# Kernel tuning notes

Measured on AMD Instinct MI355X. Metric: run time of the kernel, lower is better.

## Reference

```python
import jax, jax.numpy as jnp
import numpy as np

N_NODES = 100000
N_EDGES = 20000
NNZ = 1600000
D_IN = 128
D_OUT = 128
STAR = 64
NEG_SLOPE = 0.2


def setup_inputs() -> dict:
    key = jax.random.key(0)
    ks = jax.random.split(key, 10)
    X = jax.random.normal(ks[0], (N_NODES, D_IN), dtype=jnp.float32)
    V = jax.random.randint(ks[1], (NNZ,), 0, N_NODES, dtype=jnp.int32)
    E = jax.random.randint(ks[2], (NNZ,), 0, N_EDGES, dtype=jnp.int32)
    # guarantee full index range coverage (torch infers sizes via .max()+1)
    V = V.at[0].set(N_NODES - 1)
    E = E.at[0].set(N_EDGES - 1)
    S_features = jax.random.normal(ks[3], (N_EDGES, STAR), dtype=jnp.float32)
    # linear layer params (PyTorch convention: weight [out, in])
    def lin(k, fan_out, fan_in):
        bound = 1.0 / np.sqrt(fan_in)
        return jax.random.uniform(k, (fan_out, fan_in), jnp.float32, -bound, bound)
    Wx_w = lin(ks[4], D_OUT, D_IN)
    Wx_b = jnp.zeros((D_OUT,), jnp.float32)
    Wv_w = lin(ks[5], D_OUT, D_IN)
    Wv_b = jnp.zeros((D_OUT,), jnp.float32)
    a_w = lin(ks[6], 1, D_OUT)
    Wt_w = lin(ks[7], D_OUT, D_OUT + STAR)
    Wt_b = jnp.zeros((D_OUT,), jnp.float32)
    return {"X": X, "V": V, "E": E, "S_features": S_features,
            "Wx_w": Wx_w, "Wx_b": Wx_b, "Wv_w": Wv_w, "Wv_b": Wv_b,
            "a_w": a_w, "Wt_w": Wt_w, "Wt_b": Wt_b}


def reference(X, V, E, S_features, Wx_w, Wx_b, Wv_w, Wv_b, a_w, Wt_w, Wt_b):
    X_init = X @ Wx_w.T + Wx_b                      # [N, D_OUT]
    X_feat = X @ Wv_w.T + Wv_b                      # [N, D_OUT]
    score = (X_feat @ a_w.T)[:, 0]                  # [N]
    s = jax.nn.leaky_relu(score[V], NEG_SLOPE)      # [nnz], gather
    # scatter_softmax over hyperedge groups E
    m = jax.ops.segment_max(s, E, num_segments=N_EDGES)
    w = jnp.exp(s - m[E])
    denom = jax.ops.segment_sum(w, E, num_segments=N_EDGES)
    soft = w / denom[E]                             # [nnz]
    Xev = X_feat[V] * soft[:, None]                 # [nnz, D_OUT]
    Y_v2e = jax.nn.elu(jax.ops.segment_sum(Xev, E, num_segments=N_EDGES))
    e_msg = jnp.concatenate([Y_v2e, S_features], axis=1)  # [Eg, D_OUT+STAR]
    Y = e_msg @ Wt_w.T + Wt_b                       # [Eg, D_OUT]
    Yev = Y[E]                                      # [nnz, D_OUT]
    cnt = jax.ops.segment_sum(jnp.ones((Yev.shape[0],), X.dtype), V, num_segments=N_NODES)
    Xm = jax.ops.segment_sum(Yev, V, num_segments=N_NODES) / jnp.maximum(cnt, 1.0)[:, None]
    Xm = jax.nn.elu(Xm)  # is_last=False; dropout rate 0 -> no-op
    return Xm + X_init
```

## Files before the change

kernel.cpp:

```cpp
#include <hip/hip_runtime.h>
#include <hip/hip_bf16.h>
#include <hip/hip_fp16.h>

#define N_NODES 100000
#define N_EDGES 20000
#define NNZ     1600000
#define D       128
#define STAR    64
#define NEG_SLOPE 0.2f

#define NBLK_E  400
#define CHUNK_E 4000
#define H32_E   10000

#define NBLK_N  64
#define CHUNK_N 25000
#define BINS_N  20000
#define H32_N   10000
#define NPASS_N 5

#define NGRP    8
#define CPG_E   (NBLK_E / NGRP)
#define CPG_N   (NBLK_N / NGRP)

#define SCAT_NWG ((NNZ + 255) / 256)
#define SCAT_Q   (SCAT_NWG / 8)
#define SCAT_R   (SCAT_NWG % 8)

#define TGB_E ((N_EDGES + 255) / 256)
#define TGB_N ((N_NODES + 255) / 256)

#define SCC 16
#define SC_PER_BLOCK (256 * SCC)
#define SCB_E ((N_EDGES + SC_PER_BLOCK - 1) / SC_PER_BLOCK)
#define SCB_N ((N_NODES + SC_PER_BLOCK - 1) / SC_PER_BLOCK)

typedef _Float16 half8 __attribute__((ext_vector_type(8)));
typedef float    floatx4 __attribute__((ext_vector_type(4)));

__device__ __forceinline__ float elu_fast(float t)
{
    return (t > 0.f) ? t : (__expf(t) - 1.f);
}

__device__ __forceinline__ half8 cvt8(float4 f0, float4 f1)
{
    half8 h;
    h[0] = (_Float16)f0.x; h[1] = (_Float16)f0.y;
    h[2] = (_Float16)f0.z; h[3] = (_Float16)f0.w;
    h[4] = (_Float16)f1.x; h[5] = (_Float16)f1.y;
    h[6] = (_Float16)f1.z; h[7] = (_Float16)f1.w;
    return h;
}

__global__ __launch_bounds__(256) void k_cvt_w(
    const float* __restrict__ Wx, const float* __restrict__ Wv,
    const float* __restrict__ Wt,
    __half* __restrict__ Wf16, __half* __restrict__ Wtf16)
{
    int i = (blockIdx.x * 256 + threadIdx.x) * 4;
    const float* src;
    __half* dst;
    if (i < 16384)            { src = Wx + i;         dst = Wf16 + i; }
    else if (i < 32768)       { src = Wv + (i-16384); dst = Wf16 + i; }
    else if (i < 32768+24576) { src = Wt + (i-32768); dst = Wtf16 + (i-32768); }
    else return;
    float4 f = *(const float4*)src;
    *(__half2*)(dst)     = __floats2half2_rn(f.x, f.y);
    *(__half2*)(dst + 2) = __floats2half2_rn(f.z, f.w);
}

__global__ __launch_bounds__(256) void k_node_gemm(
    const float* __restrict__ X, const __half* __restrict__ Wf16,
    const float* __restrict__ Wxb, const float* __restrict__ Wvb,
    const float* __restrict__ aw,
    float* __restrict__ Xinit, __half* __restrict__ Xf16,
    float* __restrict__ wexp)
{
    __shared__ char smem[64 * 256];
    const int tid  = threadIdx.x;
    const int w    = tid >> 6;
    const int lane = tid & 63;
    const int bm   = blockIdx.x * 64;
    const int colbase = w * 64;
    const bool isInit = (colbase < D);
    const int r16 = lane & 15;
    const int hi  = lane >> 4;
    const int g8  = hi * 8;

    {
        const int r  = tid >> 2;
        int srow = bm + r; if (srow >= N_NODES) srow = N_NODES - 1;
        const float4* src = (const float4*)(X + (size_t)srow * D + (tid & 3) * 32);
        float4 f[8];
        #pragma unroll
        for (int j = 0; j < 8; ++j) f[j] = src[j];
        const int swz  = (r & 7) << 4;
        const int base = r * 256 + (tid & 3) * 64;
        #pragma unroll
        for (int j = 0; j < 4; ++j)
            *(half8*)(smem + ((base + j * 16) ^ swz)) = cvt8(f[2*j], f[2*j+1]);
    }

    half8 bf[4][4];
    #pragma unroll
    for (int ks = 0; ks < 4; ++ks)
        #pragma unroll
        for (int n = 0; n < 4; ++n)
            bf[ks][n] = *(const half8*)(Wf16 + (size_t)(colbase + n*16 + r16) * D
                                        + ks * 32 + g8);

    __syncthreads();

    floatx4 acc[4][4] = {};
    #pragma unroll
    for (int ks = 0; ks < 4; ++ks) {
        half8 a[4];
        #pragma unroll
        for (int m = 0; m < 4; ++m) {
            const int R = m * 16 + r16;
            a[m] = *(const half8*)(smem + ((R*256 + ks*64 + hi*16) ^ ((R&7)<<4)));
        }
        #pragma unroll
        for (int m = 0; m < 4; ++m)
            #pragma unroll
            for (int n = 0; n < 4; ++n)
                acc[m][n] = __builtin_amdgcn_mfma_f32_16x16x32_f16(
                    bf[ks][n], a[m], acc[m][n], 0, 0, 0);
    }

    const float* bias = isInit ? Wxb : Wvb;

    __syncthreads();

    if (isInit) {
        #pragma unroll
        for (int n = 0; n < 4; ++n) {
            const int c4 = (colbase & (D - 1)) + n * 16 + hi * 4;
            float4 bb = *(const float4*)(bias + c4);
            #pragma unroll
            for (int m = 0; m < 4; ++m) {
                const int row = bm + m * 16 + r16;
                if (row < N_NODES) {
                    float4 o = make_float4(acc[m][n][0] + bb.x, acc[m][n][1] + bb.y,
                                           acc[m][n][2] + bb.z, acc[m][n][3] + bb.w);
                    *(float4*)(Xinit + (size_t)row * D + c4) = o;
                }
            }
        }
    } else {
        #pragma unroll
        for (int n = 0; n < 4; ++n) {
            const int c4 = (colbase & (D - 1)) + n * 16 + hi * 4;
            float4 bb = *(const float4*)(bias + c4);
            const int lcb = ((colbase - D) + n * 16 + hi * 4) * 2;
            #pragma unroll
            for (int m = 0; m < 4; ++m) {
                const int row = m * 16 + r16;
                char* dst = smem + row * 256 + (lcb ^ ((row & 7) << 4));
                *(__half2*)(dst)     = __floats2half2_rn(acc[m][n][0] + bb.x,
                                                         acc[m][n][1] + bb.y);
                *(__half2*)(dst + 4) = __floats2half2_rn(acc[m][n][2] + bb.z,
                                                         acc[m][n][3] + bb.w);
            }
        }
    }
    __syncthreads();
    {
        const int r   = tid >> 2;
        const int row = bm + r;
        const int q4  = tid & 3;
        if (row < N_NODES) {
            const int swz = (r & 7) << 4;
            __half* dst = Xf16 + (size_t)row * D + q4 * 32;
            float part = 0.f;
            #pragma unroll
            for (int j = 0; j < 4; ++j) {
                half8 h = *(const half8*)(smem + r * 256 + ((q4 * 64 + j * 16) ^ swz));
                *(half8*)(dst + j * 8) = h;
                float4 a0 = *(const float4*)(aw + q4 * 32 + j * 8);
                float4 a1 = *(const float4*)(aw + q4 * 32 + j * 8 + 4);
                part += (float)h[0]*a0.x + (float)h[1]*a0.y
                      + (float)h[2]*a0.z + (float)h[3]*a0.w
                      + (float)h[4]*a1.x + (float)h[5]*a1.y
                      + (float)h[6]*a1.z + (float)h[7]*a1.w;
            }
            part += __shfl_xor(part, 1, 64);
            part += __shfl_xor(part, 2, 64);
            if (q4 == 0) {
                float l = (part > 0.f) ? part : NEG_SLOPE * part;
                wexp[row] = expf(l);
            }
        }
    }
}

__global__ __launch_bounds__(256) void k_part_all(
    const int* __restrict__ E, const int* __restrict__ V,
    unsigned short* __restrict__ part_e, unsigned short* __restrict__ part_n,
    unsigned short* __restrict__ re, unsigned short* __restrict__ rn)
{
    __shared__ int h[H32_E];
    const int blk = blockIdx.x;
    for (int t = threadIdx.x; t < H32_E; t += 256) h[t] = 0;
    __syncthreads();

    if (blk < NBLK_E) {
        const int b = blk;
        const int i0 = b * CHUNK_E;
        const int4* E4 = (const int4*)(E + i0);
        for (int i = threadIdx.x; i < CHUNK_E / 4; i += 256) {
            int4 q = E4[i];
            int ev[4] = {q.x, q.y, q.z, q.w};
            #pragma unroll
            for (int t = 0; t < 4; ++t) {
                int e = ev[t];
                unsigned sh = (e & 1) << 4;
                int old = atomicAdd(&h[e >> 1], 1 << sh);
                re[i0 + i * 4 + t] = (unsigned short)((unsigned)old >> sh);
            }
        }
        __syncthreads();
        int* dst = (int*)(part_e + (size_t)b * N_EDGES);
        for (int t = threadIdx.x; t < H32_E; t += 256) dst[t] = h[t];
    } else {
        const int idx = blk - NBLK_E;
        const int b   = idx & 63;
        const int c0  = (idx >> 6) * BINS_N;
        const int i0  = b * CHUNK_N;
        const int4* V4 = (const int4*)(V + i0);
        for (int i = threadIdx.x; i < CHUNK_N / 4; i += 256) {
            int4 q = V4[i];
            int vv[4] = {q.x, q.y, q.z, q.w};
            #pragma unroll
            for (int t = 0; t < 4; ++t) {
                int c = vv[t] - c0;
                if ((unsigned)c < (unsigned)BINS_N) {
                    unsigned sh = (c & 1) << 4;
                    int old = atomicAdd(&h[c >> 1], 1 << sh);
                    rn[i0 + i * 4 + t] = (unsigned short)((unsigned)old >> sh);
                }
            }
        }
        __syncthreads();
        int* dst = (int*)(part_n + (size_t)b * N_NODES + c0);
        for (int t = threadIdx.x; t < H32_N; t += 256) dst[t] = h[t];
    }
}

__global__ __launch_bounds__(256) void k_tot_grp2(
    unsigned short* __restrict__ part_e, int* __restrict__ gsum_e,
    unsigned short* __restrict__ part_n, int* __restrict__ gsum_n)
{
    const int g = blockIdx.y;
    unsigned short* part; int* gsum; int nbins, cpg, bin;
    if (blockIdx.x < TGB_E) {
        bin = blockIdx.x * 256 + threadIdx.x;
        part = part_e; gsum = gsum_e; nbins = N_EDGES; cpg = CPG_E;
    } else {
        bin = (blockIdx.x - TGB_E) * 256 + threadIdx.x;
        part = part_n; gsum = gsum_n; nbins = N_NODES; cpg = CPG_N;
    }
    if (bin >= nbins) return;
    int run = 0;
    #pragma unroll 8
    for (int b = g * cpg; b < (g + 1) * cpg; ++b) {
        size_t idx = (size_t)b * nbins + bin;
        int v = part[idx];
        part[idx] = (unsigned short)run;
        run += v;
    }
    gsum[(size_t)g * nbins + bin] = run;
}

__global__ __launch_bounds__(256) void k_tot_fin2(
    int* __restrict__ gsum_e, int* __restrict__ tot_e,
    int* __restrict__ gsum_n, int* __restrict__ tot_n)
{
    int* gsum; int* tot; int nbins, bin;
    if (blockIdx.x < TGB_E) {
        bin = blockIdx.x * 256 + threadIdx.x;
        gsum = gsum_e; tot = tot_e; nbins = N_EDGES;
    } else {
        bin = (blockIdx.x - TGB_E) * 256 + threadIdx.x;
        gsum = gsum_n; tot = tot_n; nbins = N_NODES;
    }
    if (bin >= nbins) return;
    int run = 0;
    #pragma unroll
    for (int g = 0; g < NGRP; ++g) {
        size_t idx = (size_t)g * nbins + bin;
        int v = gsum[idx];
        gsum[idx] = run;
        run += v;
    }
    tot[bin] = run;
}

__global__ __launch_bounds__(256) void k_scan_bsum2(
    const int* __restrict__ tot_e, int* __restrict__ bsum_e,
    const int* __restrict__ tot_n, int* __restrict__ bsum_n)
{
    __shared__ int red[256];
    const int* cnt; int* bsum; int n, blk;
    if (blockIdx.x < SCB_E) { cnt = tot_e; bsum = bsum_e; n = N_EDGES; blk = blockIdx.x; }
    else { cnt = tot_n; bsum = bsum_n; n = N_NODES; blk = blockIdx.x - SCB_E; }
    const int base = blk * SC_PER_BLOCK + threadIdx.x * SCC;
    int s = 0;
    if (base + SCC <= n) {
        const int4* p4 = (const int4*)(cnt + base);
        #pragma unroll
        for (int j = 0; j < SCC / 4; ++j) {
            int4 v = p4[j];
            s += v.x + v.y + v.z + v.w;
        }
    } else {
        for (int i = base; i < n; ++i) s += cnt[i];
    }
    red[threadIdx.x] = s;
    __syncthreads();
    for (int d = 128; d > 0; d >>= 1) {
        if (threadIdx.x < d) red[threadIdx.x] += red[threadIdx.x + d];
        __syncthreads();
    }
    if (threadIdx.x == 0) bsum[blk] = red[0];
}

__global__ __launch_bounds__(1024) void k_scan_bbase2(
    int* __restrict__ bsum_e, int* __restrict__ eoff,
    int* __restrict__ bsum_n, int* __restrict__ noff)
{
    __shared__ int sums[1024];
    int* bsum; int* off; int nb, n;
    if (blockIdx.x == 0) { bsum = bsum_e; off = eoff; nb = SCB_E; n = N_EDGES; }
    else                 { bsum = bsum_n; off = noff; nb = SCB_N; n = N_NODES; }
    const int tid = threadIdx.x;
    sums[tid] = (tid < nb) ? bsum[tid] : 0;
    __syncthreads();
    for (int d = 1; d < 1024; d <<= 1) {
        int mine = sums[tid];
        int other = (tid >= d) ? sums[tid - d] : 0;
        __syncthreads();
        sums[tid] = mine + other;
        __syncthreads();
    }
    if (tid < nb) bsum[tid] = (tid > 0) ? sums[tid - 1] : 0;
    if (tid == 0) off[n] = sums[1023];
}

__global__ __launch_bounds__(256) void k_scan_out2(
    const int* __restrict__ tot_e, const int* __restrict__ bsum_e,
    int* __restrict__ eoff,
    const int* __restrict__ tot_n, const int* __restrict__ bsum_n,
    int* __restrict__ noff)
{
    __shared__ int tsum[256];
    const int* cnt; const int* bsum; int* off; int n, blk;
    if (blockIdx.x < SCB_E) {
        cnt = tot_e; bsum = bsum_e; off = eoff; n = N_EDGES; blk = blockIdx.x;
    } else {
        cnt = tot_n; bsum = bsum_n; off = noff; n = N_NODES; blk = blockIdx.x - SCB_E;
    }
    const int base = blk * SC_PER_BLOCK + threadIdx.x * SCC;
    int vals[SCC];
    int s = 0;
    if (base + SCC <= n) {
        const int4* p4 = (const int4*)(cnt + base);
        #pragma unroll
        for (int j = 0; j < SCC / 4; ++j) {
            int4 v = p4[j];
            vals[4 * j + 0] = v.x; vals[4 * j + 1] = v.y;
            vals[4 * j + 2] = v.z; vals[4 * j + 3] = v.w;
            s += v.x + v.y + v.z + v.w;
        }
    } else {
        #pragma unroll
        for (int j = 0; j < SCC; ++j) {
            int i = base + j;
            vals[j] = (i < n) ? cnt[i] : 0;
            s += vals[j];
        }
    }
    tsum[threadIdx.x] = s;
    __syncthreads();
    for (int d = 1; d < 256; d <<= 1) {
        int mine = tsum[threadIdx.x];
        int other = (threadIdx.x >= d) ? tsum[threadIdx.x - d] : 0;
        __syncthreads();
        tsum[threadIdx.x] = mine + other;
        __syncthreads();
    }
    int run = bsum[blk] + ((threadIdx.x > 0) ? tsum[threadIdx.x - 1] : 0);
    #pragma unroll
    for (int j = 0; j < SCC; ++j) {
        int i = base + j;
        if (i < n) { off[i] = run; run += vals[j]; }
    }
}

__global__ __launch_bounds__(256) void k_scatter_both(
    const int* __restrict__ V, const int* __restrict__ E,
    const unsigned short* __restrict__ re, const unsigned short* __restrict__ rn,
    const unsigned short* __restrict__ part_e,
    const unsigned short* __restrict__ part_n,
    const int* __restrict__ gsum_e, const int* __restrict__ gsum_n,
    const int* __restrict__ eoff, const int* __restrict__ noff,
    int* __restrict__ epairs, unsigned short* __restrict__ nedges)
{
    const int bid = blockIdx.x;
    const int xcd = bid & 7;
    const int j   = bid >> 3;
    const int vb  = (xcd < SCAT_R) ? xcd * (SCAT_Q + 1) + j
                                   : SCAT_R * (SCAT_Q + 1) + (xcd - SCAT_R) * SCAT_Q + j;
    int i = vb * 256 + (int)threadIdx.x;
    if (i >= NNZ) return;
    int e = E[i], v = V[i];
    int be = i / CHUNK_E;
    int bn = i / CHUNK_N;
    int g  = i / 200000;
    int pe = eoff[e] + gsum_e[(size_t)g * N_EDGES + e]
                     + part_e[(size_t)be * N_EDGES + e] + re[i];
    int pn = noff[v] + gsum_n[(size_t)g * N_NODES + v]
                     + part_n[(size_t)bn * N_NODES + v] + rn[i];
    epairs[pe] = v;
    nedges[pn] = (unsigned short)e;
}

__device__ __forceinline__ void acc8h(float w, float4 raw, float (&a)[8])
{
    const __half2* h = (const __half2*)&raw;
    #pragma unroll
    for (int t = 0; t < 4; ++t) {
        float2 f = __half22float2(h[t]);
        a[2*t]   = fmaf(w, f.x, a[2*t]);
        a[2*t+1] = fmaf(w, f.y, a[2*t+1]);
    }
}

__global__ __launch_bounds__(256) void k_edge_agg(
    const int* __restrict__ epairs, const int* __restrict__ eoff,
    const float* __restrict__ wexp,
    const __half* __restrict__ Xf16, const float* __restrict__ S,
    float* __restrict__ emsg)
{
    const int wave = threadIdx.x >> 6, lane = threadIdx.x & 63;
    const int e = blockIdx.x * 4 + wave;
    if (e >= N_EDGES) return;
    const int beg = eoff[e], end = eoff[e + 1];
    const int slot = lane >> 4;
    const int sl = lane & 15;
    float a[8] = {};
    float dsum = 0.f;
    int j = beg;
    for (; j + 15 < end; j += 16) {
        int v0 = epairs[j + slot];
        int v1 = epairs[j + 4 + slot];
        int v2 = epairs[j + 8 + slot];
        int v3 = epairs[j + 12 + slot];
        float w0 = wexp[v0], w1 = wexp[v1], w2 = wexp[v2], w3 = wexp[v3];
        float4 r0 = *(const float4*)(Xf16 + (size_t)v0 * D + sl * 8);
        float4 r1 = *(const float4*)(Xf16 + (size_t)v1 * D + sl * 8);
        float4 r2 = *(const float4*)(Xf16 + (size_t)v2 * D + sl * 8);
        float4 r3 = *(const float4*)(Xf16 + (size_t)v3 * D + sl * 8);
        dsum += (w0 + w1) + (w2 + w3);
        acc8h(w0, r0, a);
        acc8h(w1, r1, a);
        acc8h(w2, r2, a);
        acc8h(w3, r3, a);
    }
    for (; j + 3 < end; j += 4) {
        int v = epairs[j + slot];
        float w = wexp[v];
        float4 r = *(const float4*)(Xf16 + (size_t)v * D + sl * 8);
        dsum += w;
        acc8h(w, r, a);
    }
    if (j + slot < end) {
        int v = epairs[j + slot];
        float w = wexp[v];
        float4 r = *(const float4*)(Xf16 + (size_t)v * D + sl * 8);
        dsum += w;
        acc8h(w, r, a);
    }
    #pragma unroll
    for (int k = 0; k < 8; ++k) {
        a[k] += __shfl_xor(a[k], 16, 64);
        a[k] += __shfl_xor(a[k], 32, 64);
    }
    dsum += __shfl_xor(dsum, 16, 64);
    dsum += __shfl_xor(dsum, 32, 64);

    float inv = (end > beg) ? 1.f / dsum : 0.f;
    float y[8];
    #pragma unroll
    for (int k = 0; k < 8; ++k)
        y[k] = elu_fast(a[k] * inv);
    const size_t rb = (size_t)e * (D + STAR);
    if (slot == 0) {
        *(float4*)(emsg + rb + sl * 8)     = make_float4(y[0], y[1], y[2], y[3]);
        *(float4*)(emsg + rb + sl * 8 + 4) = make_float4(y[4], y[5], y[6], y[7]);
    } else if (slot == 1) {
        float4 s4 = *(const float4*)(S + (size_t)e * STAR + sl * 4);
        *(float4*)(emsg + rb + D + sl * 4) = s4;
    }
}

__global__ __launch_bounds__(256) void k_edge_gemm(
    const float* __restrict__ A, const __half* __restrict__ Wtf16,
    const float* __restrict__ Wtb, __half* __restrict__ Y16)
{
    __shared__ char smem[64 * 384];
    const int KDIM = D + STAR;
    const int tid  = threadIdx.x;
    const int w    = tid >> 6;
    const int lane = tid & 63;
    const int bm   = blockIdx.x * 64;
    const int colbase = w * 32;
    const int r16 = lane & 15;
    const int hi  = lane >> 4;
    const int g8  = hi * 8;

    {
        const int r = tid >> 2;
        int srow = bm + r; if (srow >= N_EDGES) srow = N_EDGES - 1;
        const float4* src = (const float4*)(A + (size_t)srow * KDIM + (tid & 3) * 48);
        float4 f[12];
        #pragma unroll
        for (int j = 0; j < 12; ++j) f[j] = src[j];
        const int swz  = (r & 7) << 4;
        const int base = r * 384 + (tid & 3) * 96;
        #pragma unroll
        for (int j = 0; j < 6; ++j)
            *(half8*)(smem + ((base + j * 16) ^ swz)) = cvt8(f[2*j], f[2*j+1]);
    }

    half8 bf[6][2];
    #pragma unroll
    for (int ks = 0; ks < 6; ++ks)
        #pragma unroll
        for (int n = 0; n < 2; ++n)
            bf[ks][n] = *(const half8*)(Wtf16 + (size_t)(colbase + n*16 + r16) * KDIM
                                        + ks * 32 + g8);

    __syncthreads();

    floatx4 acc[4][2] = {};
    #pragma unroll
    for (int ks = 0; ks < 6; ++ks) {
        half8 a[4];
        #pragma unroll
        for (int m = 0; m < 4; ++m) {
            const int R = m * 16 + r16;
            a[m] = *(const half8*)(smem + ((R*384 + ks*64 + hi*16) ^ ((R&7)<<4)));
        }
        #pragma unroll
        for (int m = 0; m < 4; ++m)
            #pragma unroll
            for (int n = 0; n < 2; ++n)
                acc[m][n] = __builtin_amdgcn_mfma_f32_16x16x32_f16(
                    a[m], bf[ks][n], acc[m][n], 0, 0, 0);
    }

    const int rq = hi * 4;
    __syncthreads();

    {
        __half* sh = (__half*)smem;
        #pragma unroll
        for (int n = 0; n < 2; ++n) {
            const int c = colbase + n * 16 + r16;
            const float bv = Wtb[c];
            #pragma unroll
            for (int m = 0; m < 4; ++m)
                #pragma unroll
                for (int q = 0; q < 4; ++q)
                    sh[(m * 16 + rq + q) * 128 + c] =
                        __float2half(acc[m][n][q] + bv);
        }
    }
    __syncthreads();
    {
        const int r   = tid >> 2;
        const int row = bm + r;
        if (row < N_EDGES) {
            const char* src = smem + r * 256 + (tid & 3) * 64;
            __half* dst = Y16 + (size_t)row * D + (tid & 3) * 32;
            #pragma unroll
            for (int j = 0; j < 4; ++j)
                *(half8*)(dst + j * 8) = *(const half8*)(src + j * 16);
        }
    }
}

__global__ __launch_bounds__(256) void k_node_agg(
    const unsigned short* __restrict__ nedges, const int* __restrict__ noff,
    const __half* __restrict__ Y16, float* __restrict__ out)
{
    const int wave = threadIdx.x >> 6, lane = threadIdx.x & 63;
    const int v = blockIdx.x * 4 + wave;
    if (v >= N_NODES) return;
    const int beg = noff[v], end = noff[v + 1];
    const int slot = lane >> 4;
    const int sl = lane & 15;
    float a[8] = {};
    int j = beg;
    for (; j + 7 < end; j += 8) {
        int e0 = nedges[j + slot];
        int e1 = nedges[j + 4 + slot];
        float4 r0 = *(const float4*)(Y16 + (size_t)e0 * D + sl * 8);
        float4 r1 = *(const float4*)(Y16 + (size_t)e1 * D + sl * 8);
        acc8h(1.f, r0, a);
        acc8h(1.f, r1, a);
    }
    for (; j + 3 < end; j += 4) {
        int e0 = nedges[j + slot];
        float4 r = *(const float4*)(Y16 + (size_t)e0 * D + sl * 8);
        acc8h(1.f, r, a);
    }
    if (j + slot < end) {
        int e0 = nedges[j + slot];
        float4 r = *(const float4*)(Y16 + (size_t)e0 * D + sl * 8);
        acc8h(1.f, r, a);
    }
    #pragma unroll
    for (int k = 0; k < 8; ++k) {
        a[k] += __shfl_xor(a[k], 16, 64);
        a[k] += __shfl_xor(a[k], 32, 64);
    }

    if (slot == 0) {
        int cnt = end - beg;
        float invc = 1.f / (float)max(cnt, 1);
        float x[8];
        #pragma unroll
        for (int k = 0; k < 8; ++k)
            x[k] = elu_fast(a[k] * invc);
        float4* o0 = (float4*)(out + (size_t)v * D + sl * 8);
        float4* o1 = (float4*)(out + (size_t)v * D + sl * 8 + 4);
        float4 c0 = *o0, c1 = *o1;
        *o0 = make_float4(c0.x + x[0], c0.y + x[1], c0.z + x[2], c0.w + x[3]);
        *o1 = make_float4(c1.x + x[4], c1.y + x[5], c1.z + x[6], c1.w + x[7]);
    }
}

extern "C" void kernel_launch(void* const* d_in, const int* in_sizes, int n_in,
                              void* d_out, int out_size, void* d_ws, size_t ws_size,
                              hipStream_t stream)
{
    const float* X    = (const float*)d_in[0];
    const int*   V    = (const int*)  d_in[1];
    const int*   E    = (const int*)  d_in[2];
    const float* S    = (const float*)d_in[3];
    const float* Wx_w = (const float*)d_in[4];
    const float* Wx_b = (const float*)d_in[5];
    const float* Wv_w = (const float*)d_in[6];
    const float* Wv_b = (const float*)d_in[7];
    const float* a_w  = (const float*)d_in[8];
    const float* Wt_w = (const float*)d_in[9];
    const float* Wt_b = (const float*)d_in[10];
    float* out = (float*)d_out;

    char* p = (char*)d_ws;
    auto take = [&](size_t bytes) -> char* {
        char* r = p;
        p += (bytes + 255) & ~(size_t)255;
        return r;
    };

    __half* Xf16  = (__half*)take((size_t)N_NODES * D * 2);
    float*  wexp  = (float*) take((size_t)N_NODES * 4);
    unsigned short* part_e = (unsigned short*)take((size_t)NBLK_E * N_EDGES * 2);
    unsigned short* part_n = (unsigned short*)take((size_t)NBLK_N * N_NODES * 2);
    int*    gsum_e = (int*)  take((size_t)NGRP * N_EDGES * 4);
    int*    gsum_n = (int*)  take((size_t)NGRP * N_NODES * 4);
    int*    tot_e = (int*)   take((size_t)N_EDGES * 4);
    int*    tot_n = (int*)   take((size_t)N_NODES * 4);
    int*    eoff  = (int*)   take((size_t)(N_EDGES + 1) * 4);
    int*    noff  = (int*)   take((size_t)(N_NODES + 1) * 4);
    int*    bsum_e = (int*)  take((size_t)SCB_E * 4);
    int*    bsum_n = (int*)  take((size_t)SCB_N * 4);
    unsigned short* re = (unsigned short*)take((size_t)NNZ * 2);
    unsigned short* rn = (unsigned short*)take((size_t)NNZ * 2);
    int*    epairs = (int*)  take((size_t)NNZ * 4);
    unsigned short* nedges = (unsigned short*)take((size_t)NNZ * 2);
    float*  emsg  = (float*) take((size_t)N_EDGES * (D + STAR) * 4);
    __half* Y16   = (__half*)take((size_t)N_EDGES * D * 2);
    __half* Wf16  = (__half*)take((size_t)256 * D * 2);
    __half* Wtf16 = (__half*)take((size_t)D * (D + STAR) * 2);

    k_cvt_w<<<56, 256, 0, stream>>>(Wx_w, Wv_w, Wt_w, Wf16, Wtf16);

    k_node_gemm<<<(N_NODES + 63) / 64, 256, 0, stream>>>(
        X, Wf16, Wx_b, Wv_b, a_w, out, Xf16, wexp);

    k_part_all<<<NBLK_E + NBLK_N * NPASS_N, 256, 0, stream>>>(
        E, V, part_e, part_n, re, rn);

    k_tot_grp2<<<dim3(TGB_E + TGB_N, NGRP), 256, 0, stream>>>(
        part_e, gsum_e, part_n, gsum_n);
    k_tot_fin2<<<TGB_E + TGB_N, 256, 0, stream>>>(
        gsum_e, tot_e, gsum_n, tot_n);
    k_scan_bsum2<<<SCB_E + SCB_N, 256, 0, stream>>>(
        tot_e, bsum_e, tot_n, bsum_n);
    k_scan_bbase2<<<2, 1024, 0, stream>>>(bsum_e, eoff, bsum_n, noff);
    k_scan_out2<<<SCB_E + SCB_N, 256, 0, stream>>>(
        tot_e, bsum_e, eoff, tot_n, bsum_n, noff);

    k_scatter_both<<<SCAT_NWG, 256, 0, stream>>>(
        V, E, re, rn, part_e, part_n, gsum_e, gsum_n,
        eoff, noff, epairs, nedges);

    k_edge_agg<<<(N_EDGES + 3) / 4, 256, 0, stream>>>(
        epairs, eoff, wexp, Xf16, S, emsg);

    k_edge_gemm<<<(N_EDGES + 63) / 64, 256, 0, stream>>>(emsg, Wtf16, Wt_b, Y16);

    k_node_agg<<<(N_NODES + 3) / 4, 256, 0, stream>>>(nedges, noff, Y16, out);
}
```

Measured before the change: 384.1 us.

## Split edge aggregation across four feature-column quarters per edge

Each edge's 128-wide aggregation is now split across four blocks, one per 32-column quarter. Within a wave, 16 nnz slots run in parallel with 4 lanes per quarter. The block index is remapped so the four quarter-blocks of the same edges are launched close together, which should help the shared epairs/wexp reads hit in cache. This adds parallelism and shortens the per-wave serial loop. In exchange, the index and weight loads are repeated four times and the shuffle reduction grows from two steps to four.

New measurement: 426.2 us. 11.0% more time.

```diff
diff --git a/kernel.cpp b/kernel.cpp
--- a/kernel.cpp
+++ b/kernel.cpp
@@ -26,6 +26,10 @@
 #define SCAT_NWG ((NNZ + 255) / 256)
 #define SCAT_Q   (SCAT_NWG / 8)
 #define SCAT_R   (SCAT_NWG % 8)
+
+#define EAGG_EB  (N_EDGES / 4)
+#define EAGG_NWG (4 * EAGG_EB)
+#define EAGG_HB  (EAGG_EB / 2)
 
 #define TGB_E ((N_EDGES + 255) / 256)
 #define TGB_N ((N_NODES + 255) / 256)
@@ -443,65 +447,73 @@
     const __half* __restrict__ Xf16, const float* __restrict__ S,
     float* __restrict__ emsg)
 {
+    const int k  = blockIdx.x & 7;
+    const int jb = blockIdx.x >> 3;
+    const int q  = k & 3;
+    const int hh = k >> 2;
+    const int eb = hh * EAGG_HB + jb;
     const int wave = threadIdx.x >> 6, lane = threadIdx.x & 63;
-    const int e = blockIdx.x * 4 + wave;
+    const int e = eb * 4 + wave;
     if (e >= N_EDGES) return;
     const int beg = eoff[e], end = eoff[e + 1];
-    const int slot = lane >> 4;
-    const int sl = lane & 15;
+    const int slot = lane >> 2;
+    const int sl   = lane & 3;
+    const int d0   = q * 32 + sl * 8;
+
     float a[8] = {};
     float dsum = 0.f;
     int j = beg;
-    for (; j + 15 < end; j += 16) {
+    for (; j + 31 < end; j += 32) {
         int v0 = epairs[j + slot];
-        int v1 = epairs[j + 4 + slot];
-        int v2 = epairs[j + 8 + slot];
-        int v3 = epairs[j + 12 + slot];
-        float w0 = wexp[v0], w1 = wexp[v1], w2 = wexp[v2], w3 = wexp[v3];
-        float4 r0 = *(const float4*)(Xf16 + (size_t)v0 * D + sl * 8);
-        float4 r1 = *(const float4*)(Xf16 + (size_t)v1 * D + sl * 8);
-        float4 r2 = *(const float4*)(Xf16 + (size_t)v2 * D + sl * 8);
-        float4 r3 = *(const float4*)(Xf16 + (size_t)v3 * D + sl * 8);
-        dsum += (w0 + w1) + (w2 + w3);
+        int v1 = epairs[j + 16 + slot];
+        float w0 = wexp[v0], w1 = wexp[v1];
+        float4 r0 = *(const float4*)(Xf16 + (size_t)v0 * D + d0);
+        float4 r1 = *(const float4*)(Xf16 + (size_t)v1 * D + d0);
+        dsum += w0 + w1;
         acc8h(w0, r0, a);
         acc8h(w1, r1, a);
-        acc8h(w2, r2, a);
-        acc8h(w3, r3, a);
-    }
-    for (; j + 3 < end; j += 4) {
+    }
+    for (; j + 15 < end; j += 16) {
         int v = epairs[j + slot];
         float w = wexp[v];
-        float4 r = *(const float4*)(Xf16 + (size_t)v * D + sl * 8);
+        float4 r = *(const float4*)(Xf16 + (size_t)v * D + d0);
         dsum += w;
         acc8h(w, r, a);
     }
     if (j + slot < end) {
         int v = epairs[j + slot];
         float w = wexp[v];
-        float4 r = *(const float4*)(Xf16 + (size_t)v * D + sl * 8);
+        float4 r = *(const float4*)(Xf16 + (size_t)v * D + d0);
         dsum += w;
         acc8h(w, r, a);
     }
     #pragma unroll
-    for (int k = 0; k < 8; ++k) {
-        a[k] += __shfl_xor(a[k], 16, 64);
-        a[k] += __shfl_xor(a[k], 32, 64);
-    }
+    for (int t = 0; t < 8; ++t) {
+        a[t] += __shfl_xor(a[t], 4, 64);
+        a[t] += __shfl_xor(a[t], 8, 64);
+        a[t] += __shfl_xor(a[t], 16, 64);
+        a[t] += __shfl_xor(a[t], 32, 64);
+    }
+    dsum += __shfl_xor(dsum, 4, 64);
+    dsum += __shfl_xor(dsum, 8, 64);
     dsum += __shfl_xor(dsum, 16, 64);
     dsum += __shfl_xor(dsum, 32, 64);
 
     float inv = (end > beg) ? 1.f / dsum : 0.f;
     float y[8];
     #pragma unroll
-    for (int k = 0; k < 8; ++k)
-        y[k] = elu_fast(a[k] * inv);
+    for (int t = 0; t < 8; ++t)
+        y[t] = elu_fast(a[t] * inv);
     const size_t rb = (size_t)e * (D + STAR);
     if (slot == 0) {
-        *(float4*)(emsg + rb + sl * 8)     = make_float4(y[0], y[1], y[2], y[3]);
-        *(float4*)(emsg + rb + sl * 8 + 4) = make_float4(y[4], y[5], y[6], y[7]);
-    } else if (slot == 1) {
-        float4 s4 = *(const float4*)(S + (size_t)e * STAR + sl * 4);
-        *(float4*)(emsg + rb + D + sl * 4) = s4;
+        *(float4*)(emsg + rb + d0)     = make_float4(y[0], y[1], y[2], y[3]);
+        *(float4*)(emsg + rb + d0 + 4) = make_float4(y[4], y[5], y[6], y[7]);
+    } else if (slot == 1 && q >= 2) {
+        const int so = (q - 2) * 32 + sl * 8;
+        float4 s0 = *(const float4*)(S + (size_t)e * STAR + so);
+        float4 s1 = *(const float4*)(S + (size_t)e * STAR + so + 4);
+        *(float4*)(emsg + rb + D + so)     = s0;
+        *(float4*)(emsg + rb + D + so + 4) = s1;
     }
 }
 
@@ -710,7 +722,7 @@
         V, E, re, rn, part_e, part_n, gsum_e, gsum_n,
         eoff, noff, epairs, nedges);
 
-    k_edge_agg<<<(N_EDGES + 3) / 4, 256, 0, stream>>>(
+    k_edge_agg<<<EAGG_NWG, 256, 0, stream>>>(
         epairs, eoff, wexp, Xf16, S, emsg);
 
     k_edge_gemm<<<(N_EDGES + 63) / 64, 256, 0, stream>>>(emsg, Wtf16, Wt_b, Y16);
```
